# Performance work log

Hardware: AMD Instinct MI355X
Metric: run time of the kernel (lower is better)

## Reference

```python
import jax, jax.numpy as jnp
import numpy as np

N_NODES = 50000
N_EDGES = 800000
IN_FEATS = 128
N_HIDDEN = 128
N_CLASSES = 41


def setup_inputs() -> dict:
    key = jax.random.key(0)
    ks = jax.random.split(key, 8)
    x = jax.random.normal(ks[0], (N_NODES, IN_FEATS), dtype=jnp.float32)
    src = jax.random.randint(ks[1], (N_EDGES,), 0, N_NODES, dtype=jnp.int32)
    dst = jax.random.randint(ks[2], (N_EDGES,), 0, N_NODES, dtype=jnp.int32)
    # Xavier-ish init for linear weights (stored as [in, out])
    def lin(k, fan_in, fan_out):
        s = (2.0 / (fan_in + fan_out)) ** 0.5
        return jax.random.normal(k, (fan_in, fan_out), dtype=jnp.float32) * s
    return {
        "x": x, "src": src, "dst": dst,
        "W_self0": lin(ks[3], IN_FEATS, N_HIDDEN),
        "W_neigh0": lin(ks[4], IN_FEATS, N_HIDDEN),
        "b0": jnp.zeros((N_HIDDEN,), jnp.float32),
        "W_self1": lin(ks[5], N_HIDDEN, N_CLASSES),
        "W_neigh1": lin(ks[6], N_HIDDEN, N_CLASSES),
        "b1": jnp.zeros((N_CLASSES,), jnp.float32),
    }


def _sage_conv(h, src, dst, W_self, W_neigh, b, n_nodes):
    # mean aggregation over in-neighbors: gather -> segment_sum -> divide by degree
    msg = h[src]  # [E, d]
    agg = jax.ops.segment_sum(msg, dst, num_segments=n_nodes)  # [N, d]
    deg = jax.ops.segment_sum(jnp.ones((src.shape[0],), h.dtype), dst, num_segments=n_nodes)
    agg = agg / jnp.maximum(deg, 1.0)[:, None]  # zero in-degree -> 0 (DGL semantics)
    return h @ W_self + agg @ W_neigh + b


def reference(x, src, dst, W_self0, W_neigh0, b0, W_self1, W_neigh1, b1):
    n = x.shape[0]
    h = _sage_conv(x, src, dst, W_self0, W_neigh0, b0, n)
    h = jax.nn.relu(h)  # dropout is identity in eval mode
    h = _sage_conv(h, src, dst, W_self1, W_neigh1, b1, n)
    return h
```

## Files before the change

### kernel.cpp

```cpp
#include <hip/hip_runtime.h>
#include <hip/hip_bf16.h>

#define N_NODES 50000
#define N_EDGES 800000
#define F 128
#define NC 41
#define SCAN_BLK 256
#define N_SCAN_BLKS ((N_NODES + SCAN_BLK - 1) / SCAN_BLK)
#define NSLICE 8
#define SLICE_NODES (N_NODES / NSLICE)
#define FILL_BLKS_PER_SLICE 256

typedef __attribute__((ext_vector_type(4))) float f32x4;
typedef __attribute__((ext_vector_type(8))) short bf16x8;

__device__ __forceinline__ float bf2f(unsigned short u) {
    unsigned int x = ((unsigned int)u) << 16;
    return __uint_as_float(x);
}
__device__ __forceinline__ unsigned short f2bf(float f) {
    unsigned int x = __float_as_uint(f);
    unsigned int lsb = (x >> 16) & 1u;
    x += 0x7fffu + lsb;
    return (unsigned short)(x >> 16);
}

__global__ void zero_deg_kernel(int* deg) {
    int i = blockIdx.x * blockDim.x + threadIdx.x;
    if (i < N_NODES) deg[i] = 0;
}

__global__ void count_deg_kernel(const int* __restrict__ dst, int* __restrict__ deg) {
    int e = blockIdx.x * blockDim.x + threadIdx.x;
    if (e < N_EDGES) atomicAdd(&deg[dst[e]], 1);
}

__global__ __launch_bounds__(SCAN_BLK) void scan1_kernel(const int* __restrict__ deg,
                                                         int* __restrict__ local,
                                                         int* __restrict__ bsum) {
    __shared__ int buf[SCAN_BLK];
    int tid = threadIdx.x;
    int i = blockIdx.x * SCAN_BLK + tid;
    int v = (i < N_NODES) ? deg[i] : 0;
    buf[tid] = v;
    __syncthreads();
#pragma unroll
    for (int off = 1; off < SCAN_BLK; off <<= 1) {
        int t = (tid >= off) ? buf[tid - off] : 0;
        __syncthreads();
        buf[tid] += t;
        __syncthreads();
    }
    if (i < N_NODES) local[i] = buf[tid] - v;
    if (tid == SCAN_BLK - 1) bsum[blockIdx.x] = buf[tid];
}

__global__ __launch_bounds__(SCAN_BLK) void scan2_kernel(int* __restrict__ bsum,
                                                         int* __restrict__ row_ptr) {
    __shared__ int buf[SCAN_BLK];
    int tid = threadIdx.x;
    int v = (tid < N_SCAN_BLKS) ? bsum[tid] : 0;
    buf[tid] = v;
    __syncthreads();
#pragma unroll
    for (int off = 1; off < SCAN_BLK; off <<= 1) {
        int t = (tid >= off) ? buf[tid - off] : 0;
        __syncthreads();
        buf[tid] += t;
        __syncthreads();
    }
    if (tid < N_SCAN_BLKS) bsum[tid] = buf[tid] - v;
    if (tid == SCAN_BLK - 1) row_ptr[N_NODES] = buf[tid];
}

__global__ __launch_bounds__(SCAN_BLK) void scan3_kernel(const int* __restrict__ deg,
                                                         const int* __restrict__ local,
                                                         const int* __restrict__ bsum,
                                                         int* __restrict__ row_ptr,
                                                         int* __restrict__ cursor,
                                                         float* __restrict__ inv_deg) {
    int i = blockIdx.x * SCAN_BLK + threadIdx.x;
    if (i < N_NODES) {
        int rp = local[i] + bsum[blockIdx.x];
        row_ptr[i] = rp;
        cursor[i] = rp;
        inv_deg[i] = 1.0f / fmaxf((float)deg[i], 1.0f);
    }
}

__global__ __launch_bounds__(256) void fill_csr_sliced_kernel(const int* __restrict__ src,
                                                              const int* __restrict__ dst,
                                                              int* __restrict__ cursor,
                                                              int* __restrict__ csr_src) {
    int slice = blockIdx.x & (NSLICE - 1);
    int bid = blockIdx.x >> 3;
    int lo = slice * SLICE_NODES, hi = lo + SLICE_NODES;
    int stride = FILL_BLKS_PER_SLICE * 256;
    for (int e = bid * 256 + threadIdx.x; e < N_EDGES; e += stride) {
        int d = dst[e];
        if (d >= lo && d < hi) {
            int p = atomicAdd(&cursor[d], 1);
            csr_src[p] = src[e];
        }
    }
}

__global__ void pack_w0_kernel(const float* __restrict__ Ws, const float* __restrict__ Wn,
                               unsigned short* __restrict__ Bpk) {
    int i = blockIdx.x * blockDim.x + threadIdx.x;
    if (i >= 128 * 256) return;
    int j = i & 7, l = (i >> 3) & 63, kb = (i >> 9) & 3, ct = i >> 11;
    int k = kb * 32 + (l >> 4) * 8 + j;
    int c = ct * 16 + (l & 15);
    float v = (c < F) ? Ws[k * F + c] : Wn[k * F + (c - F)];
    Bpk[i] = f2bf(v);
}

__global__ void pack_w1_kernel(const float* __restrict__ Ws, const float* __restrict__ Wn,
                               unsigned short* __restrict__ Bpk) {
    int i = blockIdx.x * blockDim.x + threadIdx.x;
    if (i >= 128 * 128) return;
    int j = i & 7, l = (i >> 3) & 63, kb = (i >> 9) & 3, ct = i >> 11;
    int k = kb * 32 + (l >> 4) * 8 + j;
    int c = ct * 16 + (l & 15);
    float v = 0.0f;
    if (c < 48) { if (c < NC) v = Ws[k * NC + c]; }
    else if (c >= 64 && c < 112) { int cc = c - 64; if (cc < NC) v = Wn[k * NC + cc]; }
    Bpk[i] = f2bf(v);
}

template<bool AF32, int CT, int MODE>
__global__ __launch_bounds__(256) void gemm_mfma_kernel(const void* __restrict__ Av,
                                                        const unsigned short* __restrict__ Bpk,
                                                        int M,
                                                        unsigned short* __restrict__ outA,
                                                        unsigned short* __restrict__ outB) {
    __shared__ unsigned short As[64 * 128];
    int tid = threadIdx.x;
    int wave = tid >> 6, lane = tid & 63;
    int row0 = blockIdx.x * 64;

    if (AF32) {
        const float* A = (const float*)Av;
#pragma unroll
        for (int i = 0; i < 8; ++i) {
            int fid = tid + i * 256;
            int row = fid >> 5, c4 = (fid & 31) * 4;
            int grow = row0 + row; if (grow > M - 1) grow = M - 1;
            f32x4 v = *(const f32x4*)(A + (size_t)grow * F + c4);
            unsigned int p0 = (unsigned)f2bf(v.x) | ((unsigned)f2bf(v.y) << 16);
            unsigned int p1 = (unsigned)f2bf(v.z) | ((unsigned)f2bf(v.w) << 16);
            int idx = (row * 128 + c4) ^ ((row & 7) << 3);
            *(uint2*)&As[idx] = make_uint2(p0, p1);
        }
    } else {
        const unsigned short* A = (const unsigned short*)Av;
#pragma unroll
        for (int i = 0; i < 4; ++i) {
            int fid = tid + i * 256;
            int row = fid >> 4, c8 = (fid & 15) * 8;
            int grow = row0 + row; if (grow > M - 1) grow = M - 1;
            uint4 v = *(const uint4*)&A[(size_t)grow * F + c8];
            int idx = (row * 128 + c8) ^ ((row & 7) << 3);
            *(uint4*)&As[idx] = v;
        }
    }
    __syncthreads();

    f32x4 acc[4][CT];
#pragma unroll
    for (int m = 0; m < 4; ++m)
#pragma unroll
        for (int n = 0; n < CT; ++n) acc[m][n] = (f32x4){0.f, 0.f, 0.f, 0.f};

#pragma unroll
    for (int kb = 0; kb < 4; ++kb) {
        bf16x8 afr[4];
#pragma unroll
        for (int m = 0; m < 4; ++m) {
            int row = m * 16 + (lane & 15);
            int ke = kb * 32 + (lane >> 4) * 8;
            int idx = (row * 128 + ke) ^ ((row & 7) << 3);
            afr[m] = *(const bf16x8*)&As[idx];
        }
#pragma unroll
        for (int n = 0; n < CT; ++n) {
            int ct = wave * CT + n;
            bf16x8 bfr = *(const bf16x8*)&Bpk[((ct * 4 + kb) * 64 + lane) * 8];
#pragma unroll
            for (int m = 0; m < 4; ++m)
                acc[m][n] = __builtin_amdgcn_mfma_f32_16x16x32_bf16(afr[m], bfr, acc[m][n], 0, 0, 0);
        }
    }

#pragma unroll
    for (int m = 0; m < 4; ++m) {
#pragma unroll
        for (int i = 0; i < 4; ++i) {
            int r = row0 + m * 16 + (lane >> 4) * 4 + i;
            if (r < M) {
#pragma unroll
                for (int n = 0; n < CT; ++n) {
                    int c = (wave * CT + n) * 16 + (lane & 15);
                    unsigned short val = f2bf(acc[m][n][i]);
                    if (MODE == 0) {
                        outA[(size_t)r * (CT * 64) + c] = val;
                    } else {
                        if (c < 48) outA[(size_t)r * 48 + c] = val;
                        else if (c >= 64 && c < 112) outB[(size_t)r * 48 + (c - 64)] = val;
                    }
                }
            }
        }
    }
}

__global__ __launch_bounds__(256) void agg0_kernel(const unsigned int* __restrict__ u,
                                                   const int* __restrict__ row_ptr,
                                                   const int* __restrict__ csr_src,
                                                   const float* __restrict__ inv_deg,
                                                   const float* __restrict__ b0,
                                                   unsigned int* __restrict__ hu) {
    int node = blockIdx.x * 4 + (threadIdx.x >> 6);
    int t = threadIdx.x & 63;
    int s = row_ptr[node], e = row_ptr[node + 1];
    float ax = 0.f, ay = 0.f, bx = 0.f, by = 0.f;
    int j = s;
    for (; j + 3 < e; j += 4) {
        int sr0 = csr_src[j], sr1 = csr_src[j + 1];
        int sr2 = csr_src[j + 2], sr3 = csr_src[j + 3];
        unsigned int v0 = u[(size_t)sr0 * 128 + 64 + t];
        unsigned int v1 = u[(size_t)sr1 * 128 + 64 + t];
        unsigned int v2 = u[(size_t)sr2 * 128 + 64 + t];
        unsigned int v3 = u[(size_t)sr3 * 128 + 64 + t];
        ax += bf2f((unsigned short)(v0 & 0xffffu)) + bf2f((unsigned short)(v1 & 0xffffu));
        ay += bf2f((unsigned short)(v0 >> 16)) + bf2f((unsigned short)(v1 >> 16));
        bx += bf2f((unsigned short)(v2 & 0xffffu)) + bf2f((unsigned short)(v3 & 0xffffu));
        by += bf2f((unsigned short)(v2 >> 16)) + bf2f((unsigned short)(v3 >> 16));
    }
    for (; j < e; ++j) {
        int sr = csr_src[j];
        unsigned int v = u[(size_t)sr * 128 + 64 + t];
        ax += bf2f((unsigned short)(v & 0xffffu));
        ay += bf2f((unsigned short)(v >> 16));
    }
    ax += bx; ay += by;
    float inv = inv_deg[node];
    unsigned int vs = u[(size_t)node * 128 + t];
    float2 bb = ((const float2*)b0)[t];
    float h0 = fmaxf(bf2f((unsigned short)(vs & 0xffffu)) + ax * inv + bb.x, 0.0f);
    float h1 = fmaxf(bf2f((unsigned short)(vs >> 16)) + ay * inv + bb.y, 0.0f);
    hu[(size_t)node * 64 + t] = (unsigned)f2bf(h0) | ((unsigned)f2bf(h1) << 16);
}

__global__ __launch_bounds__(256) void final_out_kernel(const unsigned int* __restrict__ ts,
                                                        const unsigned int* __restrict__ tn,
                                                        const int* __restrict__ row_ptr,
                                                        const int* __restrict__ csr_src,
                                                        const float* __restrict__ inv_deg,
                                                        const float* __restrict__ b1,
                                                        float* __restrict__ out) {
    int node = blockIdx.x * 4 + (threadIdx.x >> 6);
    int lane = threadIdx.x & 63;
    int group = lane >> 5;
    int c = lane & 31;
    int s = row_ptr[node], e = row_ptr[node + 1];
    float ax = 0.f, ay = 0.f, bx = 0.f, by = 0.f;
    int j = s + group;
    for (; j + 6 < e; j += 8) {
        int sr0 = csr_src[j], sr1 = csr_src[j + 2];
        int sr2 = csr_src[j + 4], sr3 = csr_src[j + 6];
        unsigned int v0 = tn[(size_t)sr0 * 24 + c];
        unsigned int v1 = tn[(size_t)sr1 * 24 + c];
        unsigned int v2 = tn[(size_t)sr2 * 24 + c];
        unsigned int v3 = tn[(size_t)sr3 * 24 + c];
        ax += bf2f((unsigned short)(v0 & 0xffffu)) + bf2f((unsigned short)(v1 & 0xffffu));
        ay += bf2f((unsigned short)(v0 >> 16)) + bf2f((unsigned short)(v1 >> 16));
        bx += bf2f((unsigned short)(v2 & 0xffffu)) + bf2f((unsigned short)(v3 & 0xffffu));
        by += bf2f((unsigned short)(v2 >> 16)) + bf2f((unsigned short)(v3 >> 16));
    }
    for (; j < e; j += 2) {
        int sr = csr_src[j];
        unsigned int v = tn[(size_t)sr * 24 + c];
        ax += bf2f((unsigned short)(v & 0xffffu));
        ay += bf2f((unsigned short)(v >> 16));
    }
    ax += bx; ay += by;
    ax += __shfl(ax, lane + 32, 64);
    ay += __shfl(ay, lane + 32, 64);
    if (lane >= 24) return;
    float inv = inv_deg[node];
    unsigned int vs = ts[(size_t)node * 24 + c];
    int c0 = 2 * c, c1 = 2 * c + 1;
    if (c0 < NC)
        out[(size_t)node * NC + c0] = bf2f((unsigned short)(vs & 0xffffu)) + b1[c0] + ax * inv;
    if (c1 < NC)
        out[(size_t)node * NC + c1] = bf2f((unsigned short)(vs >> 16)) + b1[c1] + ay * inv;
}

extern "C" void kernel_launch(void* const* d_in, const int* in_sizes, int n_in,
                              void* d_out, int out_size, void* d_ws, size_t ws_size,
                              hipStream_t stream) {
    const float* x   = (const float*)d_in[0];
    const int*   src = (const int*)d_in[1];
    const int*   dst = (const int*)d_in[2];
    const float* Ws0 = (const float*)d_in[3];
    const float* Wn0 = (const float*)d_in[4];
    const float* b0  = (const float*)d_in[5];
    const float* Ws1 = (const float*)d_in[6];
    const float* Wn1 = (const float*)d_in[7];
    const float* b1  = (const float*)d_in[8];
    float* out = (float*)d_out;

    char* ws = (char*)d_ws;
    size_t o = 0;
    auto alloc = [&](size_t bytes) {
        size_t r = o;
        o = (o + bytes + 255) & ~(size_t)255;
        return r;
    };
    int*   deg     = (int*)(ws + alloc(sizeof(int) * N_NODES));
    int*   local   = (int*)(ws + alloc(sizeof(int) * N_NODES));
    int*   bsum    = (int*)(ws + alloc(sizeof(int) * N_SCAN_BLKS));
    int*   row_ptr = (int*)(ws + alloc(sizeof(int) * (N_NODES + 1)));
    int*   cursor  = (int*)(ws + alloc(sizeof(int) * N_NODES));
    int*   csr     = (int*)(ws + alloc(sizeof(int) * N_EDGES));
    float* inv_deg = (float*)(ws + alloc(sizeof(float) * N_NODES));
    unsigned short* Bpk0 = (unsigned short*)(ws + alloc(sizeof(short) * 128 * 256));
    unsigned short* Bpk1 = (unsigned short*)(ws + alloc(sizeof(short) * 128 * 128));
    unsigned short* u    = (unsigned short*)(ws + alloc(sizeof(short) * (size_t)N_NODES * 256));
    unsigned short* h    = (unsigned short*)(ws + alloc(sizeof(short) * (size_t)N_NODES * 128));
    unsigned short* t_self  = (unsigned short*)(ws + alloc(sizeof(short) * (size_t)N_NODES * 48));
    unsigned short* t_neigh = (unsigned short*)(ws + alloc(sizeof(short) * ((size_t)N_NODES * 48 + 128)));

    zero_deg_kernel<<<(N_NODES + 255) / 256, 256, 0, stream>>>(deg);
    count_deg_kernel<<<(N_EDGES + 255) / 256, 256, 0, stream>>>(dst, deg);
    scan1_kernel<<<N_SCAN_BLKS, SCAN_BLK, 0, stream>>>(deg, local, bsum);
    scan2_kernel<<<1, SCAN_BLK, 0, stream>>>(bsum, row_ptr);
    scan3_kernel<<<N_SCAN_BLKS, SCAN_BLK, 0, stream>>>(deg, local, bsum, row_ptr, cursor, inv_deg);
    fill_csr_sliced_kernel<<<NSLICE * FILL_BLKS_PER_SLICE, 256, 0, stream>>>(src, dst, cursor, csr);
    pack_w0_kernel<<<(128 * 256 + 255) / 256, 256, 0, stream>>>(Ws0, Wn0, Bpk0);
    pack_w1_kernel<<<(128 * 128 + 255) / 256, 256, 0, stream>>>(Ws1, Wn1, Bpk1);

    int nblk = (N_NODES + 63) / 64;
    gemm_mfma_kernel<true, 4, 0><<<nblk, 256, 0, stream>>>(x, Bpk0, N_NODES, u, nullptr);
    agg0_kernel<<<N_NODES / 4, 256, 0, stream>>>((const unsigned int*)u, row_ptr, csr, inv_deg, b0,
                                                 (unsigned int*)h);
    gemm_mfma_kernel<false, 2, 1><<<nblk, 256, 0, stream>>>(h, Bpk1, N_NODES, t_self, t_neigh);
    final_out_kernel<<<N_NODES / 4, 256, 0, stream>>>((const unsigned int*)t_self,
                                                      (const unsigned int*)t_neigh,
                                                      row_ptr, csr, inv_deg, b1, out);
}
```

Baseline: 262.6 us.

## Slice degree counting, merge weight packing, deepen gather unroll in aggregation kernels

Degree counting now uses the same slice-partitioned scheme as the CSR fill, so each block group's atomics hit one node range for better L2 locality. The zeroing kernel is replaced by a memset, and the two weight-pack kernels are merged into one launch. The neighbor-gather loops in both aggregation kernels are unrolled from 4 to 8 loads to keep more memory requests in flight. The trade-offs are that every edge's dst is read 8 times during counting, and the deeper unroll raises register pressure.

```diff
diff --git a/kernel.cpp b/kernel.cpp
--- a/kernel.cpp
+++ b/kernel.cpp
@@ -25,14 +25,16 @@
     return (unsigned short)(x >> 16);
 }
 
-__global__ void zero_deg_kernel(int* deg) {
-    int i = blockIdx.x * blockDim.x + threadIdx.x;
-    if (i < N_NODES) deg[i] = 0;
-}
-
-__global__ void count_deg_kernel(const int* __restrict__ dst, int* __restrict__ deg) {
-    int e = blockIdx.x * blockDim.x + threadIdx.x;
-    if (e < N_EDGES) atomicAdd(&deg[dst[e]], 1);
+__global__ __launch_bounds__(256) void count_deg_sliced_kernel(const int* __restrict__ dst,
+                                                               int* __restrict__ deg) {
+    int slice = blockIdx.x & (NSLICE - 1);
+    int bid = blockIdx.x >> 3;
+    int lo = slice * SLICE_NODES, hi = lo + SLICE_NODES;
+    int stride = FILL_BLKS_PER_SLICE * 256;
+    for (int e = bid * 256 + threadIdx.x; e < N_EDGES; e += stride) {
+        int d = dst[e];
+        if (d >= lo && d < hi) atomicAdd(&deg[d], 1);
+    }
 }
 
 __global__ __launch_bounds__(SCAN_BLK) void scan1_kernel(const int* __restrict__ deg,
@@ -105,28 +107,27 @@
     }
 }
 
-__global__ void pack_w0_kernel(const float* __restrict__ Ws, const float* __restrict__ Wn,
-                               unsigned short* __restrict__ Bpk) {
+__global__ void pack_w_kernel(const float* __restrict__ Ws0, const float* __restrict__ Wn0,
+                              const float* __restrict__ Ws1, const float* __restrict__ Wn1,
+                              unsigned short* __restrict__ Bpk0,
+                              unsigned short* __restrict__ Bpk1) {
     int i = blockIdx.x * blockDim.x + threadIdx.x;
-    if (i >= 128 * 256) return;
-    int j = i & 7, l = (i >> 3) & 63, kb = (i >> 9) & 3, ct = i >> 11;
-    int k = kb * 32 + (l >> 4) * 8 + j;
-    int c = ct * 16 + (l & 15);
-    float v = (c < F) ? Ws[k * F + c] : Wn[k * F + (c - F)];
-    Bpk[i] = f2bf(v);
-}
-
-__global__ void pack_w1_kernel(const float* __restrict__ Ws, const float* __restrict__ Wn,
-                               unsigned short* __restrict__ Bpk) {
-    int i = blockIdx.x * blockDim.x + threadIdx.x;
-    if (i >= 128 * 128) return;
-    int j = i & 7, l = (i >> 3) & 63, kb = (i >> 9) & 3, ct = i >> 11;
-    int k = kb * 32 + (l >> 4) * 8 + j;
-    int c = ct * 16 + (l & 15);
-    float v = 0.0f;
-    if (c < 48) { if (c < NC) v = Ws[k * NC + c]; }
-    else if (c >= 64 && c < 112) { int cc = c - 64; if (cc < NC) v = Wn[k * NC + cc]; }
-    Bpk[i] = f2bf(v);
+    if (i < 128 * 256) {
+        int j = i & 7, l = (i >> 3) & 63, kb = (i >> 9) & 3, ct = i >> 11;
+        int k = kb * 32 + (l >> 4) * 8 + j;
+        int c = ct * 16 + (l & 15);
+        float v = (c < F) ? Ws0[k * F + c] : Wn0[k * F + (c - F)];
+        Bpk0[i] = f2bf(v);
+    } else if (i < 128 * 256 + 128 * 128) {
+        int i2 = i - 128 * 256;
+        int j = i2 & 7, l = (i2 >> 3) & 63, kb = (i2 >> 9) & 3, ct = i2 >> 11;
+        int k = kb * 32 + (l >> 4) * 8 + j;
+        int c = ct * 16 + (l & 15);
+        float v = 0.0f;
+        if (c < 48) { if (c < NC) v = Ws1[k * NC + c]; }
+        else if (c >= 64 && c < 112) { int cc = c - 64; if (cc < NC) v = Wn1[k * NC + cc]; }
+        Bpk1[i2] = f2bf(v);
+    }
 }
 
 template<bool AF32, int CT, int MODE>
@@ -226,17 +227,27 @@
     int s = row_ptr[node], e = row_ptr[node + 1];
     float ax = 0.f, ay = 0.f, bx = 0.f, by = 0.f;
     int j = s;
-    for (; j + 3 < e; j += 4) {
-        int sr0 = csr_src[j], sr1 = csr_src[j + 1];
+    for (; j + 7 < e; j += 8) {
+        int sr0 = csr_src[j],     sr1 = csr_src[j + 1];
         int sr2 = csr_src[j + 2], sr3 = csr_src[j + 3];
+        int sr4 = csr_src[j + 4], sr5 = csr_src[j + 5];
+        int sr6 = csr_src[j + 6], sr7 = csr_src[j + 7];
         unsigned int v0 = u[(size_t)sr0 * 128 + 64 + t];
         unsigned int v1 = u[(size_t)sr1 * 128 + 64 + t];
         unsigned int v2 = u[(size_t)sr2 * 128 + 64 + t];
         unsigned int v3 = u[(size_t)sr3 * 128 + 64 + t];
+        unsigned int v4 = u[(size_t)sr4 * 128 + 64 + t];
+        unsigned int v5 = u[(size_t)sr5 * 128 + 64 + t];
+        unsigned int v6 = u[(size_t)sr6 * 128 + 64 + t];
+        unsigned int v7 = u[(size_t)sr7 * 128 + 64 + t];
         ax += bf2f((unsigned short)(v0 & 0xffffu)) + bf2f((unsigned short)(v1 & 0xffffu));
         ay += bf2f((unsigned short)(v0 >> 16)) + bf2f((unsigned short)(v1 >> 16));
         bx += bf2f((unsigned short)(v2 & 0xffffu)) + bf2f((unsigned short)(v3 & 0xffffu));
         by += bf2f((unsigned short)(v2 >> 16)) + bf2f((unsigned short)(v3 >> 16));
+        ax += bf2f((unsigned short)(v4 & 0xffffu)) + bf2f((unsigned short)(v5 & 0xffffu));
+        ay += bf2f((unsigned short)(v4 >> 16)) + bf2f((unsigned short)(v5 >> 16));
+        bx += bf2f((unsigned short)(v6 & 0xffffu)) + bf2f((unsigned short)(v7 & 0xffffu));
+        by += bf2f((unsigned short)(v6 >> 16)) + bf2f((unsigned short)(v7 >> 16));
     }
     for (; j < e; ++j) {
         int sr = csr_src[j];
@@ -267,17 +278,27 @@
     int s = row_ptr[node], e = row_ptr[node + 1];
     float ax = 0.f, ay = 0.f, bx = 0.f, by = 0.f;
     int j = s + group;
-    for (; j + 6 < e; j += 8) {
-        int sr0 = csr_src[j], sr1 = csr_src[j + 2];
-        int sr2 = csr_src[j + 4], sr3 = csr_src[j + 6];
+    for (; j + 14 < e; j += 16) {
+        int sr0 = csr_src[j],      sr1 = csr_src[j + 2];
+        int sr2 = csr_src[j + 4],  sr3 = csr_src[j + 6];
+        int sr4 = csr_src[j + 8],  sr5 = csr_src[j + 10];
+        int sr6 = csr_src[j + 12], sr7 = csr_src[j + 14];
         unsigned int v0 = tn[(size_t)sr0 * 24 + c];
         unsigned int v1 = tn[(size_t)sr1 * 24 + c];
         unsigned int v2 = tn[(size_t)sr2 * 24 + c];
         unsigned int v3 = tn[(size_t)sr3 * 24 + c];
+        unsigned int v4 = tn[(size_t)sr4 * 24 + c];
+        unsigned int v5 = tn[(size_t)sr5 * 24 + c];
+        unsigned int v6 = tn[(size_t)sr6 * 24 + c];
+        unsigned int v7 = tn[(size_t)sr7 * 24 + c];
         ax += bf2f((unsigned short)(v0 & 0xffffu)) + bf2f((unsigned short)(v1 & 0xffffu));
         ay += bf2f((unsigned short)(v0 >> 16)) + bf2f((unsigned short)(v1 >> 16));
         bx += bf2f((unsigned short)(v2 & 0xffffu)) + bf2f((unsigned short)(v3 & 0xffffu));
         by += bf2f((unsigned short)(v2 >> 16)) + bf2f((unsigned short)(v3 >> 16));
+        ax += bf2f((unsigned short)(v4 & 0xffffu)) + bf2f((unsigned short)(v5 & 0xffffu));
+        ay += bf2f((unsigned short)(v4 >> 16)) + bf2f((unsigned short)(v5 >> 16));
+        bx += bf2f((unsigned short)(v6 & 0xffffu)) + bf2f((unsigned short)(v7 & 0xffffu));
+        by += bf2f((unsigned short)(v6 >> 16)) + bf2f((unsigned short)(v7 >> 16));
     }
     for (; j < e; j += 2) {
         int sr = csr_src[j];
@@ -333,14 +354,14 @@
     unsigned short* t_self  = (unsigned short*)(ws + alloc(sizeof(short) * (size_t)N_NODES * 48));
     unsigned short* t_neigh = (unsigned short*)(ws + alloc(sizeof(short) * ((size_t)N_NODES * 48 + 128)));
 
-    zero_deg_kernel<<<(N_NODES + 255) / 256, 256, 0, stream>>>(deg);
-    count_deg_kernel<<<(N_EDGES + 255) / 256, 256, 0, stream>>>(dst, deg);
+    hipMemsetAsync(deg, 0, sizeof(int) * N_NODES, stream);
+    count_deg_sliced_kernel<<<NSLICE * FILL_BLKS_PER_SLICE, 256, 0, stream>>>(dst, deg);
     scan1_kernel<<<N_SCAN_BLKS, SCAN_BLK, 0, stream>>>(deg, local, bsum);
     scan2_kernel<<<1, SCAN_BLK, 0, stream>>>(bsum, row_ptr);
     scan3_kernel<<<N_SCAN_BLKS, SCAN_BLK, 0, stream>>>(deg, local, bsum, row_ptr, cursor, inv_deg);
     fill_csr_sliced_kernel<<<NSLICE * FILL_BLKS_PER_SLICE, 256, 0, stream>>>(src, dst, cursor, csr);
-    pack_w0_kernel<<<(128 * 256 + 255) / 256, 256, 0, stream>>>(Ws0, Wn0, Bpk0);
-    pack_w1_kernel<<<(128 * 128 + 255) / 256, 256, 0, stream>>>(Ws1, Wn1, Bpk1);
+    pack_w_kernel<<<(128 * 256 + 128 * 128 + 255) / 256, 256, 0, stream>>>(Ws0, Wn0, Ws1, Wn1,
+                                                                           Bpk0, Bpk1);
 
     int nblk = (N_NODES + 63) / 64;
     gemm_mfma_kernel<true, 4, 0><<<nblk, 256, 0, stream>>>(x, Bpk0, N_NODES, u, nullptr);
```

Measured after the change: 263.4 us. Within noise of the previous version (+0.3%).
